# Performance work log

Measured on AMD Instinct MI355X. Metric: run time of the kernel, lower is better.

## Reference

```python
import jax, jax.numpy as jnp
import numpy as np

B, NQ, NK, DM, H, DK = 8, 1024, 1024, 512, 8, 64


def setup_inputs() -> dict:
    key = jax.random.key(0)
    ks = jax.random.split(key, 20)
    s = 1.0 / np.sqrt(DM)
    inp = {
        "queries": jax.random.normal(ks[0], (B, NQ, DM), jnp.float32),
        "keys": jax.random.normal(ks[1], (B, NK, DM), jnp.float32),
        "values": jax.random.normal(ks[2], (B, NK, DM), jnp.float32),
        "attention_mask": jax.random.randint(ks[3], (B, H, NQ, NK), 0, 2).astype(bool),
        "attention_weights": jax.random.uniform(ks[4], (B, H, NQ, NK), jnp.float32),
        "memory": jax.random.uniform(ks[5], (B, NK), jnp.float32),
        "geometry": jax.random.uniform(ks[6], (B, H, NQ, NK), jnp.float32),
        "Wq": jax.random.normal(ks[7], (DM, H * DK), jnp.float32) * s,
        "bq": jnp.zeros((H * DK,), jnp.float32),
        "Wk": jax.random.normal(ks[8], (DM, H * DK), jnp.float32) * s,
        "bk": jnp.zeros((H * DK,), jnp.float32),
        "Wv": jax.random.normal(ks[9], (DM, H * DK), jnp.float32) * s,
        "bv": jnp.zeros((H * DK,), jnp.float32),
        "Wmm": jax.random.normal(ks[10], (1, H * DK), jnp.float32),
        "bmm": jnp.zeros((H * DK,), jnp.float32),
        "Wo": jax.random.normal(ks[11], (H * DK, DM), jnp.float32) * s,
        "bo": jnp.zeros((DM,), jnp.float32),
    }
    return inp


def reference(queries, keys, values, attention_mask, attention_weights, memory,
              geometry, Wq, bq, Wk, bk, Wv, bv, Wmm, bmm, Wo, bo):
    b, nq = queries.shape[:2]
    nk = keys.shape[1]
    # projections -> (b, h, n, d)
    q = (queries @ Wq + bq).reshape(b, nq, H, DK).transpose(0, 2, 1, 3)
    k = (keys @ Wk + bk).reshape(b, nk, H, DK).transpose(0, 2, 1, 3)
    v = (values @ Wv + bv).reshape(b, nk, H, DK).transpose(0, 2, 1, 3)
    # memory gate: (b, nk, 1) @ (1, h*dk) -> (b, h, nk, dk)
    mm = (memory[..., None] @ Wmm + bmm).reshape(b, nk, H, DK).transpose(0, 2, 1, 3)
    # gated scores (b, h, nq, nk)
    att = jnp.einsum('bhqd,bhkd->bhqk', q, k * mm) / np.sqrt(DK)
    att = att * attention_weights
    att = jnp.where(attention_mask, -jnp.inf, att)
    # geometric log-bias + softmax
    w_mn = jax.nn.softmax(jnp.log(jnp.clip(geometry, 1e-6)) + att, axis=-1)
    out = jnp.einsum('bhqk,bhkd->bhqd', w_mn, v * mm)
    out = out.transpose(0, 2, 1, 3).reshape(b, nq, H * DK)
    return out @ Wo + bo
```

## Files before the change

### kernel.cpp

```cpp
#include <hip/hip_runtime.h>
#include <hip/hip_bf16.h>
#include <math.h>

#define B_ 8
#define NQ_ 1024
#define NK_ 1024
#define H_ 8
#define DK_ 64
#define HDK_ 512
#define LOG2E 1.4426950408889634f

typedef _Float16 half8 __attribute__((ext_vector_type(8)));
typedef _Float16 half4 __attribute__((ext_vector_type(4)));
typedef float f32x4 __attribute__((ext_vector_type(4)));

__global__ __launch_bounds__(256)
void wtrans_kernel(const float* __restrict__ w0, const float* __restrict__ w1,
                   const float* __restrict__ w2, const float* __restrict__ w3,
                   _Float16* __restrict__ t0, _Float16* __restrict__ t1,
                   _Float16* __restrict__ t2, _Float16* __restrict__ t3,
                   const unsigned int* __restrict__ maskw, int nwords,
                   int* __restrict__ flag) {
  __shared__ float tile[64][65];
  if (blockIdx.x == 64) {
    if (blockIdx.y != 0) return;
    __shared__ int s;
    if (threadIdx.x == 0) s = 0;
    __syncthreads();
    int bad = 0;
    for (int i = threadIdx.x; i < nwords; i += blockDim.x) {
      unsigned int v = maskw[i];
      if (v > 1u && v != 0x3F800000u) bad = 1;
    }
    if (bad) atomicOr(&s, 1);
    __syncthreads();
    if (threadIdx.x == 0) *flag = s;
    return;
  }
  const float* W;
  _Float16* T;
  switch (blockIdx.y) {
    case 0: W = w0; T = t0; break;
    case 1: W = w1; T = t1; break;
    case 2: W = w2; T = t2; break;
    default: W = w3; T = t3; break;
  }
  const int t = blockIdx.x;
  const int k0 = (t >> 3) * 64, n0 = (t & 7) * 64;
  const int tid = threadIdx.x;
  const int r = tid >> 4, c4 = (tid & 15) * 4;
#pragma unroll
  for (int i = 0; i < 4; ++i) {
    const int kk = r + i * 16;
    float4 v = *(const float4*)(W + (size_t)(k0 + kk) * 512 + n0 + c4);
    tile[kk][c4 + 0] = v.x;
    tile[kk][c4 + 1] = v.y;
    tile[kk][c4 + 2] = v.z;
    tile[kk][c4 + 3] = v.w;
  }
  __syncthreads();
#pragma unroll
  for (int i = 0; i < 4; ++i) {
    const int nn = r + i * 16;
    half4 h;
#pragma unroll
    for (int j = 0; j < 4; ++j) h[j] = (_Float16)tile[c4 + j][nn];
    *(half4*)(T + (size_t)(n0 + nn) * 512 + k0 + c4) = h;
  }
}

__global__ __launch_bounds__(256)
void gemm_kernel(const float* __restrict__ A0, const float* __restrict__ A1,
                 const float* __restrict__ A2, const _Float16* __restrict__ A16,
                 const _Float16* __restrict__ B0, const _Float16* __restrict__ B1,
                 const _Float16* __restrict__ B2, const float* __restrict__ bias0,
                 const float* __restrict__ bias1, const float* __restrict__ bias2,
                 const float* __restrict__ mem, const float* __restrict__ Wmm,
                 const float* __restrict__ bmm, void* __restrict__ out0,
                 void* __restrict__ out1, void* __restrict__ out2,
                 const int mode_base) {
  __shared__ _Float16 As[128 * 32];
  __shared__ _Float16 Bs[128 * 32];
  const int mode = mode_base + blockIdx.z;
  const float* A32 = (mode == 1) ? A1 : (mode == 2) ? A2 : A0;
  const _Float16* Bt = (mode == 1) ? B1 : (mode == 2) ? B2 : B0;
  const float* bias = (mode == 1) ? bias1 : (mode == 2) ? bias2 : bias0;
  void* outp = (mode == 1) ? out1 : (mode == 2) ? out2 : out0;

  const int tid = threadIdx.x;
  const int lane = tid & 63, wave = tid >> 6;
  const int wr = wave >> 1, wc = wave & 1;
  const int l15 = lane & 15, l4 = lane >> 4;
  const int row0 = blockIdx.x * 128, col0 = blockIdx.y * 128;
  const int srow = tid >> 1;
  const int sc0 = (tid & 1) * 2;

  f32x4 acc[4][4] = {};

  for (int k0 = 0; k0 < 512; k0 += 32) {
    __syncthreads();
    const _Float16* sb = Bt + (size_t)(col0 + srow) * 512 + k0;
#pragma unroll
    for (int c = 0; c < 2; ++c) {
      int ci = sc0 + c;
      half8 ha;
      if (mode == 3) {
        ha = *(const half8*)(A16 + (size_t)(row0 + srow) * 512 + k0 + ci * 8);
      } else {
        const float* s = A32 + (size_t)(row0 + srow) * 512 + k0 + ci * 8;
        float4 x = *(const float4*)s;
        float4 y = *(const float4*)(s + 4);
        ha[0] = (_Float16)x.x; ha[1] = (_Float16)x.y;
        ha[2] = (_Float16)x.z; ha[3] = (_Float16)x.w;
        ha[4] = (_Float16)y.x; ha[5] = (_Float16)y.y;
        ha[6] = (_Float16)y.z; ha[7] = (_Float16)y.w;
      }
      float4 vb = *(const float4*)(sb + ci * 8);
      int cd = ci ^ (srow & 3);
      *(half8*)((char*)As + srow * 64 + (cd << 4)) = ha;
      *(float4*)((char*)Bs + srow * 64 + (cd << 4)) = vb;
    }
    __syncthreads();
    half8 af[4], bf[4];
#pragma unroll
    for (int mi = 0; mi < 4; ++mi) {
      int r = wr * 64 + mi * 16 + l15;
      af[mi] = *(half8*)((char*)As + r * 64 + ((l4 ^ (r & 3)) << 4));
    }
#pragma unroll
    for (int ni = 0; ni < 4; ++ni) {
      int r = wc * 64 + ni * 16 + l15;
      bf[ni] = *(half8*)((char*)Bs + r * 64 + ((l4 ^ (r & 3)) << 4));
    }
#pragma unroll
    for (int mi = 0; mi < 4; ++mi)
#pragma unroll
      for (int ni = 0; ni < 4; ++ni)
        acc[mi][ni] =
            __builtin_amdgcn_mfma_f32_16x16x32_f16(af[mi], bf[ni], acc[mi][ni], 0, 0, 0);
  }

#pragma unroll
  for (int mi = 0; mi < 4; ++mi) {
#pragma unroll
    for (int ni = 0; ni < 4; ++ni) {
      const int gc = col0 + wc * 64 + ni * 16 + l15;
      const float bi = bias[gc];
      const int h = gc >> 6, d = gc & 63;
#pragma unroll
      for (int reg = 0; reg < 4; ++reg) {
        const int gr = row0 + wr * 64 + mi * 16 + l4 * 4 + reg;
        float val = acc[mi][ni][reg] + bi;
        if (mode == 3) {
          ((float*)outp)[(size_t)gr * 512 + gc] = val;
        } else if (mode == 0) {
          const int b = gr >> 10, n = gr & 1023;
          ((_Float16*)outp)[((size_t)(b * 8 + h) * 1024 + n) * 64 + d] =
              (_Float16)(val * (LOG2E / 8.0f));
        } else {
          const int b = gr >> 10, n = gr & 1023;
          float mmv = fmaf(mem[gr], Wmm[gc], bmm[gc]);
          float g = val * mmv;
          if (mode == 1)
            ((_Float16*)outp)[((size_t)(b * 8 + h) * 1024 + n) * 64 + d] = (_Float16)g;
          else
            ((_Float16*)outp)[((size_t)(b * 8 + h) * 64 + d) * 1024 + n] = (_Float16)g;
        }
      }
    }
  }
}

__global__ __launch_bounds__(256, 2)
void attn_kernel(const _Float16* __restrict__ Qp, const _Float16* __restrict__ Kg,
                 const _Float16* __restrict__ Vgt, const float* __restrict__ attw,
                 const float* __restrict__ geom, const void* __restrict__ maskp,
                 const int* __restrict__ flagp, _Float16* __restrict__ Ocat) {
  __shared__ _Float16 Kw[4][64 * 64];
  __shared__ _Float16 Vw[4][64 * 64];
  __shared__ _Float16 Ps[4][16 * 64];

  const int tid = threadIdx.x;
  const int lane = tid & 63, wave = tid >> 6;
  const int l15 = lane & 15, l4 = lane >> 4;
  const int bid = blockIdx.x;
  const int qt = bid >> 6;
  const int g = bid & 63;
  const int h = g & 7, b = g >> 3;
  const int bh = b * H_ + h;
  const int qb = qt * 64 + wave * 16;
  const int kq = qb + l15;
  const int maskBytes = *flagp;
  const unsigned char* m8 = (const unsigned char*)maskp;
  const int* m32 = (const int*)maskp;

  half8 aq[2];
  {
    const _Float16* qsrc = Qp + ((size_t)bh * NQ_ + kq) * DK_;
#pragma unroll
    for (int s = 0; s < 2; ++s) aq[s] = *(const half8*)(qsrc + s * 32 + l4 * 8);
  }

  f32x4 fo[4] = {};
  float mrun = -INFINITY, lrun = 0.f;

  const _Float16* Kbase = Kg + (size_t)bh * NK_ * DK_;
  const _Float16* Vbase = Vgt + (size_t)bh * DK_ * NK_;
  const size_t wgBase = ((size_t)bh << 20) + (size_t)kq * NK_ + l4 * 4;

  char* const KwB = (char*)&Kw[wave][0];
  char* const VwB = (char*)&Vw[wave][0];
  const int srow = lane >> 3;
  const int schk = lane & 7;

  half8 kreg[8], vreg[8];
  auto loadKreg = [&](int kt) {
    const _Float16* kp = Kbase + (size_t)(kt * 64) * DK_;
#pragma unroll
    for (int i = 0; i < 8; ++i)
      kreg[i] = *(const half8*)(kp + (size_t)(i * 8 + srow) * DK_ + schk * 8);
  };
  auto writeK = [&]() {
#pragma unroll
    for (int i = 0; i < 8; ++i) {
      const int r = i * 8 + srow;
      *(half8*)(KwB + r * 128 + ((schk ^ (r & 7)) << 4)) = kreg[i];
    }
  };
  auto loadVreg = [&](int kt) {
    const _Float16* vp = Vbase + kt * 64;
#pragma unroll
    for (int i = 0; i < 8; ++i)
      vreg[i] = *(const half8*)(vp + (size_t)(i * 8 + srow) * NK_ + schk * 8);
  };
  auto writeV = [&]() {
#pragma unroll
    for (int i = 0; i < 8; ++i) {
      const int r = i * 8 + srow;
      *(half8*)(VwB + r * 128 + ((schk ^ (r & 7)) << 4)) = vreg[i];
    }
  };

  float4 wv[4], gv[4];
  unsigned mk;
  auto loadWG = [&](int kt) {
    const size_t base = wgBase + (size_t)kt * 64;
    unsigned m = 0;
#pragma unroll
    for (int c = 0; c < 4; ++c) {
      wv[c] = *(const float4*)(attw + base + c * 16);
      gv[c] = *(const float4*)(geom + base + c * 16);
      if (maskBytes) {
        unsigned v = *(const unsigned*)(m8 + base + c * 16);
        m |= (((v & 0xffu) ? 1u : 0u) | ((v & 0xff00u) ? 2u : 0u) |
              ((v & 0xff0000u) ? 4u : 0u) | ((v & 0xff000000u) ? 8u : 0u)) << (c * 4);
      } else {
        int4 v = *(const int4*)(m32 + base + c * 16);
        m |= ((v.x ? 1u : 0u) | (v.y ? 2u : 0u) | (v.z ? 4u : 0u) | (v.w ? 8u : 0u))
             << (c * 4);
      }
    }
    mk = m;
  };

  loadKreg(0);
  loadVreg(0);
  loadWG(0);
  writeK();
  writeV();

  for (int kt = 0; kt < 16; ++kt) {
    if (kt + 1 < 16) {
      loadKreg(kt + 1);
      __builtin_amdgcn_sched_barrier(0);
    }

    f32x4 sf[4];
    __builtin_amdgcn_s_setprio(1);
#pragma unroll
    for (int c = 0; c < 4; ++c) {
      sf[c] = (f32x4){0.f, 0.f, 0.f, 0.f};
#pragma unroll
      for (int s = 0; s < 2; ++s) {
        int r = c * 16 + l15;
        half8 ak = *(half8*)(KwB + r * 128 + (((s * 4 + l4) ^ (r & 7)) << 4));
        sf[c] = __builtin_amdgcn_mfma_f32_16x16x32_f16(ak, aq[s], sf[c], 0, 0, 0);
      }
    }
    __builtin_amdgcn_s_setprio(0);

    if (kt + 1 < 16) {
      writeK();
      loadVreg(kt + 1);
      __builtin_amdgcn_sched_barrier(0);
    }

    float mx = -INFINITY;
#pragma unroll
    for (int c = 0; c < 4; ++c)
#pragma unroll
      for (int reg = 0; reg < 4; ++reg) {
        float sv = sf[c][reg] * wv[c][reg];
        sf[c][reg] = sv;
        mx = fmaxf(mx, sv);
      }
    mx = fmaxf(mx, __shfl_xor(mx, 16));
    mx = fmaxf(mx, __shfl_xor(mx, 32));
    const float mn = fmaxf(mrun, mx);
    const float sc = (mrun == -INFINITY) ? 0.f : exp2f(mrun - mn);
    mrun = mn;

    float rs = 0.f;
#pragma unroll
    for (int c = 0; c < 4; ++c)
#pragma unroll
      for (int reg = 0; reg < 4; ++reg) {
        float p = fmaxf(gv[c][reg], 1e-6f) * exp2f(sf[c][reg] - mn);
        p = ((mk >> (c * 4 + reg)) & 1u) ? 0.f : p;
        sf[c][reg] = p;
        rs += p;
      }

    if (kt + 1 < 16) {
      loadWG(kt + 1);
      __builtin_amdgcn_sched_barrier(0);
    }

#pragma unroll
    for (int c = 0; c < 4; ++c)
#pragma unroll
      for (int reg = 0; reg < 4; ++reg) fo[c][reg] *= sc;
    lrun = lrun * sc + rs;

    char* pw = (char*)&Ps[wave][0];
#pragma unroll
    for (int c = 0; c < 4; ++c) {
      half4 hp;
#pragma unroll
      for (int reg = 0; reg < 4; ++reg) hp[reg] = (_Float16)sf[c][reg];
      int ci = c * 2 + (l4 >> 1);
      *(half4*)(pw + l15 * 128 + ((ci ^ (l15 & 7)) << 4) + (l4 & 1) * 8) = hp;
    }

    __builtin_amdgcn_s_setprio(1);
#pragma unroll
    for (int s4 = 0; s4 < 2; ++s4) {
      half8 pa = *(half8*)(pw + l15 * 128 + (((s4 * 4 + l4) ^ (l15 & 7)) << 4));
#pragma unroll
      for (int c = 0; c < 4; ++c) {
        int rd = c * 16 + l15;
        half8 bv = *(half8*)(VwB + rd * 128 + (((s4 * 4 + l4) ^ (rd & 7)) << 4));
        fo[c] = __builtin_amdgcn_mfma_f32_16x16x32_f16(bv, pa, fo[c], 0, 0, 0);
      }
    }
    __builtin_amdgcn_s_setprio(0);

    if (kt + 1 < 16) writeV();
  }

  float lsum = lrun;
  lsum += __shfl_xor(lsum, 16);
  lsum += __shfl_xor(lsum, 32);
  const float rinv = 1.0f / lsum;

  _Float16* orow = Ocat + ((size_t)b * NQ_ + kq) * HDK_ + h * DK_;
#pragma unroll
  for (int c = 0; c < 4; ++c) {
    half4 hv;
#pragma unroll
    for (int reg = 0; reg < 4; ++reg) hv[reg] = (_Float16)(fo[c][reg] * rinv);
    *(half4*)(orow + c * 16 + l4 * 4) = hv;
  }
}

extern "C" void kernel_launch(void* const* d_in, const int* in_sizes, int n_in,
                              void* d_out, int out_size, void* d_ws, size_t ws_size,
                              hipStream_t stream) {
  (void)in_sizes; (void)n_in; (void)out_size; (void)ws_size;
  const float* queries = (const float*)d_in[0];
  const float* keys    = (const float*)d_in[1];
  const float* values  = (const float*)d_in[2];
  const void*  maskp   = d_in[3];
  const float* attw    = (const float*)d_in[4];
  const float* memo    = (const float*)d_in[5];
  const float* geom    = (const float*)d_in[6];
  const float* Wq = (const float*)d_in[7];
  const float* bq = (const float*)d_in[8];
  const float* Wk = (const float*)d_in[9];
  const float* bk = (const float*)d_in[10];
  const float* Wv = (const float*)d_in[11];
  const float* bv = (const float*)d_in[12];
  const float* Wmm = (const float*)d_in[13];
  const float* bmm = (const float*)d_in[14];
  const float* Wo = (const float*)d_in[15];
  const float* bo = (const float*)d_in[16];

  char* ws = (char*)d_ws;
  size_t off = 0;
  auto alloc = [&](size_t bytes) {
    char* p = ws + off;
    off += (bytes + 255) & ~(size_t)255;
    return p;
  };
  const size_t MAT = (size_t)8192 * 512 * 2;
  int* flag = (int*)alloc(256);
  _Float16* Wtq = (_Float16*)alloc((size_t)512 * 512 * 2);
  _Float16* Wtk = (_Float16*)alloc((size_t)512 * 512 * 2);
  _Float16* Wtv = (_Float16*)alloc((size_t)512 * 512 * 2);
  _Float16* Wto = (_Float16*)alloc((size_t)512 * 512 * 2);
  _Float16* Qp   = (_Float16*)alloc(MAT);
  _Float16* Kgp  = (_Float16*)alloc(MAT);
  _Float16* Vgtp = (_Float16*)alloc(MAT);
  _Float16* Ocat = (_Float16*)alloc(MAT);

  wtrans_kernel<<<dim3(65, 4), 256, 0, stream>>>(Wq, Wk, Wv, Wo, Wtq, Wtk, Wtv, Wto,
                                                 (const unsigned int*)maskp, 4096, flag);

  gemm_kernel<<<dim3(64, 4, 3), 256, 0, stream>>>(
      queries, keys, values, nullptr, Wtq, Wtk, Wtv, bq, bk, bv, memo, Wmm, bmm,
      Qp, Kgp, Vgtp, 0);

  attn_kernel<<<1024, 256, 0, stream>>>(Qp, Kgp, Vgtp, attw, geom, maskp, flag, Ocat);

  gemm_kernel<<<dim3(64, 4, 1), 256, 0, stream>>>(
      nullptr, nullptr, nullptr, Ocat, Wto, nullptr, nullptr, bo, nullptr, nullptr,
      nullptr, nullptr, nullptr, d_out, nullptr, nullptr, 3);
}
```

Before: 321.3 us.

## Stage K/V tiles directly into LDS with async global_load_lds

Replaces the register-staged K and V tile loads (global load into registers, then an LDS write) with direct global-to-LDS loads. The XOR swizzle moves to the source addresses so the LDS layout matches what the MFMA reads expect. Explicit vmcnt/lgkmcnt waits now order the tile loads against the attention-weight, geometry and mask loads, and the kt loop is fully unrolled. The P scratch buffer switches from a swizzle to row padding of 144 bytes. This frees the 16 half8 staging registers and drops the separate LDS write pass, but correctness now depends on hand-counted outstanding-load waits being right.

```diff
diff --git a/kernel.cpp b/kernel.cpp
--- a/kernel.cpp
+++ b/kernel.cpp
@@ -176,9 +176,9 @@
                  const _Float16* __restrict__ Vgt, const float* __restrict__ attw,
                  const float* __restrict__ geom, const void* __restrict__ maskp,
                  const int* __restrict__ flagp, _Float16* __restrict__ Ocat) {
-  __shared__ _Float16 Kw[4][64 * 64];
-  __shared__ _Float16 Vw[4][64 * 64];
-  __shared__ _Float16 Ps[4][16 * 64];
+  __shared__ char Kw[4][64 * 128];
+  __shared__ char Vw[4][64 * 128];
+  __shared__ char Pw[4][16 * 144];
 
   const int tid = threadIdx.x;
   const int lane = tid & 63, wave = tid >> 6;
@@ -204,40 +204,33 @@
   f32x4 fo[4] = {};
   float mrun = -INFINITY, lrun = 0.f;
 
-  const _Float16* Kbase = Kg + (size_t)bh * NK_ * DK_;
-  const _Float16* Vbase = Vgt + (size_t)bh * DK_ * NK_;
+  const char* Kbase = (const char*)(Kg + (size_t)bh * NK_ * DK_);
+  const char* Vbase = (const char*)(Vgt + (size_t)bh * DK_ * NK_);
   const size_t wgBase = ((size_t)bh << 20) + (size_t)kq * NK_ + l4 * 4;
 
-  char* const KwB = (char*)&Kw[wave][0];
-  char* const VwB = (char*)&Vw[wave][0];
-  const int srow = lane >> 3;
-  const int schk = lane & 7;
-
-  half8 kreg[8], vreg[8];
-  auto loadKreg = [&](int kt) {
-    const _Float16* kp = Kbase + (size_t)(kt * 64) * DK_;
-#pragma unroll
-    for (int i = 0; i < 8; ++i)
-      kreg[i] = *(const half8*)(kp + (size_t)(i * 8 + srow) * DK_ + schk * 8);
+  char* const KwB = &Kw[wave][0];
+  char* const VwB = &Vw[wave][0];
+  char* const PwB = &Pw[wave][0];
+
+  const int srow8 = lane >> 3;
+  const int sc8 = lane & 7;
+
+  auto stageK = [&](int kt) {
+    const char* kgb = Kbase + (size_t)(kt * 64) * 128;
+#pragma unroll
+    for (int i = 0; i < 8; ++i) {
+      const int r = i * 8 + srow8;
+      const char* src = kgb + (size_t)r * 128 + ((sc8 ^ (r & 7)) << 4);
+      __builtin_amdgcn_global_load_lds(src, KwB + i * 1024, 16, 0, 0);
+    }
   };
-  auto writeK = [&]() {
+  auto stageV = [&](int kt) {
+    const char* vgb = Vbase + (size_t)kt * 128;
 #pragma unroll
     for (int i = 0; i < 8; ++i) {
-      const int r = i * 8 + srow;
-      *(half8*)(KwB + r * 128 + ((schk ^ (r & 7)) << 4)) = kreg[i];
-    }
-  };
-  auto loadVreg = [&](int kt) {
-    const _Float16* vp = Vbase + kt * 64;
-#pragma unroll
-    for (int i = 0; i < 8; ++i)
-      vreg[i] = *(const half8*)(vp + (size_t)(i * 8 + srow) * NK_ + schk * 8);
-  };
-  auto writeV = [&]() {
-#pragma unroll
-    for (int i = 0; i < 8; ++i) {
-      const int r = i * 8 + srow;
-      *(half8*)(VwB + r * 128 + ((schk ^ (r & 7)) << 4)) = vreg[i];
+      const int r = i * 8 + srow8;
+      const char* src = vgb + (size_t)r * (NK_ * 2) + ((sc8 ^ (r & 7)) << 4);
+      __builtin_amdgcn_global_load_lds(src, VwB + i * 1024, 16, 0, 0);
     }
   };
 
@@ -263,17 +256,14 @@
     mk = m;
   };
 
-  loadKreg(0);
-  loadVreg(0);
+  stageK(0);
   loadWG(0);
-  writeK();
-  writeV();
-
+  stageV(0);
+
+#pragma unroll
   for (int kt = 0; kt < 16; ++kt) {
-    if (kt + 1 < 16) {
-      loadKreg(kt + 1);
-      __builtin_amdgcn_sched_barrier(0);
-    }
+    asm volatile("s_waitcnt vmcnt(20)" ::: "memory");
+    __builtin_amdgcn_sched_barrier(0);
 
     f32x4 sf[4];
     __builtin_amdgcn_s_setprio(1);
@@ -290,10 +280,18 @@
     __builtin_amdgcn_s_setprio(0);
 
     if (kt + 1 < 16) {
-      writeK();
-      loadVreg(kt + 1);
+      asm volatile("s_waitcnt lgkmcnt(0)" ::: "memory");
       __builtin_amdgcn_sched_barrier(0);
-    }
+      stageK(kt + 1);
+      __builtin_amdgcn_sched_barrier(0);
+    }
+
+    if (kt + 1 < 16) {
+      asm volatile("s_waitcnt vmcnt(16)" ::: "memory");
+    } else {
+      asm volatile("s_waitcnt vmcnt(8)" ::: "memory");
+    }
+    __builtin_amdgcn_sched_barrier(0);
 
     float mx = -INFINITY;
 #pragma unroll
@@ -332,20 +330,25 @@
       for (int reg = 0; reg < 4; ++reg) fo[c][reg] *= sc;
     lrun = lrun * sc + rs;
 
-    char* pw = (char*)&Ps[wave][0];
 #pragma unroll
     for (int c = 0; c < 4; ++c) {
       half4 hp;
 #pragma unroll
       for (int reg = 0; reg < 4; ++reg) hp[reg] = (_Float16)sf[c][reg];
-      int ci = c * 2 + (l4 >> 1);
-      *(half4*)(pw + l15 * 128 + ((ci ^ (l15 & 7)) << 4) + (l4 & 1) * 8) = hp;
-    }
+      *(half4*)(PwB + l15 * 144 + c * 32 + l4 * 8) = hp;
+    }
+
+    if (kt + 1 < 16) {
+      asm volatile("s_waitcnt vmcnt(20)" ::: "memory");
+    } else {
+      asm volatile("s_waitcnt vmcnt(0)" ::: "memory");
+    }
+    __builtin_amdgcn_sched_barrier(0);
 
     __builtin_amdgcn_s_setprio(1);
 #pragma unroll
     for (int s4 = 0; s4 < 2; ++s4) {
-      half8 pa = *(half8*)(pw + l15 * 128 + (((s4 * 4 + l4) ^ (l15 & 7)) << 4));
+      half8 pa = *(half8*)(PwB + l15 * 144 + s4 * 64 + l4 * 16);
 #pragma unroll
       for (int c = 0; c < 4; ++c) {
         int rd = c * 16 + l15;
@@ -355,7 +358,12 @@
     }
     __builtin_amdgcn_s_setprio(0);
 
-    if (kt + 1 < 16) writeV();
+    if (kt + 1 < 16) {
+      asm volatile("s_waitcnt lgkmcnt(0)" ::: "memory");
+      __builtin_amdgcn_sched_barrier(0);
+      stageV(kt + 1);
+      __builtin_amdgcn_sched_barrier(0);
+    }
   }
 
   float lsum = lrun;
```

New measurement: 400.2 us. +24.6%, slower.
